# Optimization experiments

Measured on AMD Instinct MI355X. Metric: run time of the kernel, lower is better.

The kernel has to match this reference:

```python
import jax, jax.numpy as jnp
import numpy as np

N_SEG = 64        # number of graphs in batch
NEG_SLOPE = 0.2   # PyG GATConv leaky_relu slope


def seg_softmax(vals, seg, num_segments):
    # vals: [E, H]; softmax over entries sharing the same segment id
    m = jax.ops.segment_max(vals, seg, num_segments=num_segments)
    m = jnp.where(jnp.isfinite(m), m, 0.0)  # guard empty segments
    e = jnp.exp(vals - m[seg])
    s = jax.ops.segment_sum(e, seg, num_segments=num_segments)
    return e / (s[seg] + 1e-16)


def setup_inputs() -> dict:
    key = jax.random.key(0)
    ks = jax.random.split(key, 16)
    N, E, Fin, H, C1, C2 = 50000, 800000, 128, 4, 32, 128
    x = jax.random.normal(ks[0], (N, Fin), jnp.float32)
    edge_index = jax.random.randint(ks[1], (2, E), 0, N)
    batch = jnp.sort(jax.random.randint(ks[2], (N,), 0, N_SEG))
    sc = lambda fan: 1.0 / np.sqrt(fan)
    W_gat = jax.random.normal(ks[3], (Fin, H * C1), jnp.float32) * sc(Fin)
    att_src = jax.random.normal(ks[4], (H, C1), jnp.float32) * sc(C1)
    att_dst = jax.random.normal(ks[5], (H, C1), jnp.float32) * sc(C1)
    b_gat = jnp.zeros((H * C1,), jnp.float32)
    bn1_w = jax.random.uniform(ks[6], (H * C1,), jnp.float32, 0.5, 1.5)
    bn1_b = jax.random.normal(ks[7], (H * C1,), jnp.float32) * 0.1
    W_gcn = jax.random.normal(ks[8], (H * C1, C2), jnp.float32) * sc(H * C1)
    b_gcn = jnp.zeros((C2,), jnp.float32)
    bn2_w = jax.random.uniform(ks[9], (C2,), jnp.float32, 0.5, 1.5)
    bn2_b = jax.random.normal(ks[10], (C2,), jnp.float32) * 0.1
    W_gate = jax.random.normal(ks[11], (C2, 1), jnp.float32) * sc(C2)
    b_gate = jnp.zeros((1,), jnp.float32)
    W_fc = jax.random.normal(ks[12], (C2, 1), jnp.float32) * sc(C2)
    b_fc = jnp.zeros((1,), jnp.float32)
    return dict(x=x, edge_index=edge_index, batch=batch, W_gat=W_gat,
                att_src=att_src, att_dst=att_dst, b_gat=b_gat,
                bn1_w=bn1_w, bn1_b=bn1_b, W_gcn=W_gcn, b_gcn=b_gcn,
                bn2_w=bn2_w, bn2_b=bn2_b, W_gate=W_gate, b_gate=b_gate,
                W_fc=W_fc, b_fc=b_fc)


def reference(x, edge_index, batch, W_gat, att_src, att_dst, b_gat,
              bn1_w, bn1_b, W_gcn, b_gcn, bn2_w, bn2_b,
              W_gate, b_gate, W_fc, b_fc):
    N = x.shape[0]
    H, C1 = att_src.shape
    loops = jnp.arange(N)
    src = jnp.concatenate([edge_index[0], loops])  # message source j
    dst = jnp.concatenate([edge_index[1], loops])  # aggregation target i

    # ---- GATConv (heads=4, concat, add_self_loops) ----
    h = (x @ W_gat).reshape(N, H, C1)                       # [N,H,C1]
    a_src = jnp.einsum('nhc,hc->nh', h, att_src)
    a_dst = jnp.einsum('nhc,hc->nh', h, att_dst)
    e = jax.nn.leaky_relu(a_src[src] + a_dst[dst], NEG_SLOPE)  # [E',H]
    alpha = seg_softmax(e, dst, N)
    msg = h[src] * alpha[..., None]                          # [E',H,C1]
    out1 = jax.ops.segment_sum(msg, dst, num_segments=N).reshape(N, H * C1) + b_gat
    out1 = jax.nn.elu(out1)
    out1 = out1 * bn1_w + bn1_b          # BatchNorm1d (eval: mean 0, var 1)
    # dropout: identity (eval mode)

    # ---- GCNConv (self-loops, symmetric normalization) ----
    deg = jax.ops.segment_sum(jnp.ones_like(dst, dtype=x.dtype), dst, num_segments=N)
    dinv = jax.lax.rsqrt(jnp.maximum(deg, 1.0))
    norm = dinv[src] * dinv[dst]                             # [E']
    h2 = out1 @ W_gcn                                        # [N,C2]
    out2 = jax.ops.segment_sum(h2[src] * norm[:, None], dst, num_segments=N) + b_gcn
    out2 = jax.nn.elu(out2)
    out2 = out2 * bn2_w + bn2_b

    # ---- GlobalAttention pooling ----
    gate = out2 @ W_gate + b_gate                            # [N,1]
    w = seg_softmax(gate, batch, N_SEG)
    graph_rep = jax.ops.segment_sum(w * out2, batch, num_segments=N_SEG)  # [G,C2]

    out = graph_rep @ W_fc + b_fc                            # [G,1]
    return out.squeeze(1)
```

## Files before the change

kernel.cpp:

```cpp
#include <hip/hip_runtime.h>
#include <math.h>


#define NEG_SLOPE 0.2f
#define BKT_BITS 7
#define BKT_SIZE 128
#define CHUNK_A 4096

typedef __attribute__((ext_vector_type(8))) short short8v;
typedef __attribute__((ext_vector_type(4))) float floatx4;

__device__ __forceinline__ int lower_bound_i(const int* a, int n, int key) {
    int lo = 0, hi = n;
    while (lo < hi) {
        int mid = (lo + hi) >> 1;
        if (a[mid] < key) lo = mid + 1; else hi = mid;
    }
    return lo;
}

__device__ __forceinline__ unsigned pack_bf16(float lo, float hi) {
    unsigned ua = __float_as_uint(lo);
    unsigned ub = __float_as_uint(hi);
    ua = ua + 0x7fffu + ((ua >> 16) & 1u);
    ub = ub + 0x7fffu + ((ub >> 16) & 1u);
    return (ua >> 16) | (ub & 0xffff0000u);
}

__device__ __forceinline__ unsigned short bf16_1(float v) {
    unsigned u = __float_as_uint(v);
    u = u + 0x7fffu + ((u >> 16) & 1u);
    return (unsigned short)(u >> 16);
}

__global__ __launch_bounds__(256) void k_front(
    const float* __restrict__ W1, const float* __restrict__ atts,
    const float* __restrict__ attd, const float* __restrict__ W2,
    unsigned short* __restrict__ Wt1, unsigned short* __restrict__ Wt2,
    const int* __restrict__ dst, int* __restrict__ bcount, int E, int NB)
{
    const int b = blockIdx.x;
    if (b < 2) {
        const float* W = b ? W2 : W1;
        unsigned short* Wt = b ? Wt2 : Wt1;
        const int lim = b ? (128 * 128) : (144 * 128);
        for (int idx = threadIdx.x; idx < lim; idx += 256) {
            int j = idx >> 7, i = idx & 127;
            float v;
            if (j < 128) v = W[i * 128 + j];
            else if (j < 132) {
                int h = j - 128; float s = 0.f;
                for (int c = 0; c < 32; c++) s += W1[i * 128 + h * 32 + c] * atts[h * 32 + c];
                v = s;
            } else if (j < 136) {
                int h = j - 132; float s = 0.f;
                for (int c = 0; c < 32; c++) s += W1[i * 128 + h * 32 + c] * attd[h * 32 + c];
                v = s;
            } else v = 0.f;
            Wt[idx] = bf16_1(v);
        }
    } else {
        __shared__ int h[512];
        const int tid = threadIdx.x;
        for (int i = tid; i < 512; i += 256) h[i] = 0;
        __syncthreads();
        int base = (b - 2) * 2048;
#pragma unroll
        for (int k = 0; k < 8; k++) {
            int e = base + k * 256 + tid;
            if (e < E) atomicAdd(&h[dst[e] >> BKT_BITS], 1);
        }
        __syncthreads();
        for (int i = tid; i < NB; i += 256) {
            int c = h[i];
            if (c) atomicAdd(&bcount[i], c);
        }
    }
}

template<int MODE>
__global__ __launch_bounds__(256) void k_gemm_mfma(
    const void* __restrict__ Ain, const unsigned short* __restrict__ Wt,
    unsigned* __restrict__ Cb, int N,
    const float* __restrict__ pb, const float* __restrict__ pw,
    const float* __restrict__ pb2, const float* __restrict__ dinv,
    float* __restrict__ aS, float* __restrict__ aD)
{
    constexpr int NCT = (MODE == 0) ? 9 : 8;
    __shared__ unsigned short sA[128 * 136];
    __shared__ unsigned short sB[NCT * 16 * 136];
    const int tid = threadIdx.x;
    const int n0 = blockIdx.x * 128;

    {
        const uint4* Wg = (const uint4*)Wt;
        const int nq = NCT * 16 * 16;
        for (int q = tid; q < nq; q += 256) {
            uint4 v = Wg[q];
            int j = q >> 4, seg = q & 15;
            *(uint4*)(sB + j * 136 + seg * 8) = v;
        }
    }
    if (MODE == 0) {
        const float* A = (const float*)Ain;
        const int w4 = tid & 31;
        const int r0 = tid >> 5;
#pragma unroll
        for (int i = 0; i < 16; i++) {
            int r = r0 + 8 * i;
            int gn = n0 + r;
            unsigned p0 = 0, p1 = 0;
            if (gn < N) {
                float4 v = *(const float4*)(A + (size_t)gn * 128 + w4 * 4);
                p0 = pack_bf16(v.x, v.y);
                p1 = pack_bf16(v.z, v.w);
            }
            *(uint2*)(sA + r * 136 + w4 * 4) = make_uint2(p0, p1);
        }
    } else {
        const unsigned short* A = (const unsigned short*)Ain;
        const int w8 = tid & 15;
        const int r0 = tid >> 4;
        const int k0 = w8 * 8;
        float pbv[8], pwv[8], p2v[8];
        *(float4*)(pbv)     = *(const float4*)(pb + k0);
        *(float4*)(pbv + 4) = *(const float4*)(pb + k0 + 4);
        *(float4*)(pwv)     = *(const float4*)(pw + k0);
        *(float4*)(pwv + 4) = *(const float4*)(pw + k0 + 4);
        *(float4*)(p2v)     = *(const float4*)(pb2 + k0);
        *(float4*)(p2v + 4) = *(const float4*)(pb2 + k0 + 4);
#pragma unroll
        for (int i = 0; i < 8; i++) {
            int r = r0 + 16 * i;
            int gn = n0 + r;
            uint4 outv = make_uint4(0, 0, 0, 0);
            if (gn < N) {
                uint4 v = *(const uint4*)(A + (size_t)gn * 128 + k0);
                unsigned uu[4] = {v.x, v.y, v.z, v.w};
                unsigned ro[4];
#pragma unroll
                for (int q2 = 0; q2 < 4; q2++) {
                    float lo = __uint_as_float(uu[q2] << 16);
                    float hi = __uint_as_float(uu[q2] & 0xffff0000u);
                    float t;
                    t = lo + pbv[2 * q2];     t = (t > 0.f) ? t : expm1f(t); lo = t * pwv[2 * q2]     + p2v[2 * q2];
                    t = hi + pbv[2 * q2 + 1]; t = (t > 0.f) ? t : expm1f(t); hi = t * pwv[2 * q2 + 1] + p2v[2 * q2 + 1];
                    ro[q2] = pack_bf16(lo, hi);
                }
                outv = make_uint4(ro[0], ro[1], ro[2], ro[3]);
            }
            *(uint4*)(sA + r * 136 + k0) = outv;
        }
    }
    __syncthreads();

    const int wid = tid >> 6, lane = tid & 63;
    const int quad = lane >> 4, l16 = lane & 15;

    floatx4 acc[2][NCT];
#pragma unroll
    for (int rt = 0; rt < 2; rt++)
#pragma unroll
        for (int ct = 0; ct < NCT; ct++) acc[rt][ct] = (floatx4){0.f, 0.f, 0.f, 0.f};

    const unsigned short* pa0 = sA + (wid * 32 + l16) * 136 + quad * 8;
    const unsigned short* pbt = sB + l16 * 136 + quad * 8;
#pragma unroll
    for (int ks = 0; ks < 4; ks++) {
        short8v a0 = *(const short8v*)(pa0 + ks * 32);
        short8v a1 = *(const short8v*)(pa0 + 16 * 136 + ks * 32);
#pragma unroll
        for (int ct = 0; ct < NCT; ct++) {
            short8v bv = *(const short8v*)(pbt + ct * (16 * 136) + ks * 32);
            acc[0][ct] = __builtin_amdgcn_mfma_f32_16x16x32_bf16(a0, bv, acc[0][ct], 0, 0, 0);
            acc[1][ct] = __builtin_amdgcn_mfma_f32_16x16x32_bf16(a1, bv, acc[1][ct], 0, 0, 0);
        }
    }

#pragma unroll
    for (int rt = 0; rt < 2; rt++) {
#pragma unroll
        for (int r = 0; r < 4; r++) {
            int n = n0 + wid * 32 + rt * 16 + quad * 4 + r;
            if (n >= N) continue;
            float s = MODE ? dinv[n] : 1.f;
#pragma unroll
            for (int ct = 0; ct < 4; ct++) {
                Cb[(size_t)n * 64 + ct * 16 + l16] =
                    pack_bf16(acc[rt][ct][r] * s, acc[rt][ct + 4][r] * s);
            }
            if (MODE == 0) {
                float e = acc[rt][8][r];
                if (l16 < 4) aS[(size_t)n * 4 + l16] = e;
                else if (l16 < 8) aD[(size_t)n * 4 + (l16 - 4)] = e;
            }
        }
    }
}

__global__ __launch_bounds__(512) void k_bscan(const int* __restrict__ bcount,
                                               int* __restrict__ bb,
                                               int* __restrict__ bcur, int NB)
{
    __shared__ int sc[512];
    const int tid = threadIdx.x;
    int own = (tid < NB) ? bcount[tid] : 0;
    sc[tid] = own;
    __syncthreads();
    for (int st = 1; st < 512; st <<= 1) {
        int v = 0;
        if (tid >= st) v = sc[tid - st];
        __syncthreads();
        if (tid >= st) sc[tid] += v;
        __syncthreads();
    }
    int excl = sc[tid] - own;
    if (tid < NB) { bb[tid] = excl; bcur[tid] = excl; }
    if (tid == 511) { bb[NB] = sc[511]; bcur[NB] = sc[511]; }
}

__global__ __launch_bounds__(256) void k_binA(const int* __restrict__ ei,
                                              int* __restrict__ bcur,
                                              int2* __restrict__ pairs,
                                              int E, int NB)
{
    __shared__ int h[512];
    __shared__ int base[512];
    const int tid = threadIdx.x;
    for (int i = tid; i < NB + 1; i += 256) h[i] = 0;
    __syncthreads();
    const int c0 = blockIdx.x * CHUNK_A;
    int s[16], d[16], b[16];
#pragma unroll
    for (int k = 0; k < 16; k++) {
        int e = c0 + k * 256 + tid;
        bool v = e < E;
        s[k] = v ? ei[e] : 0;
        d[k] = v ? ei[E + e] : 0;
        b[k] = v ? (d[k] >> BKT_BITS) : NB;
        atomicAdd(&h[b[k]], 1);
    }
    __syncthreads();
    for (int i = tid; i < NB + 1; i += 256) {
        int c = h[i];
        base[i] = c ? atomicAdd(&bcur[i], c) : 0;
        h[i] = 0;
    }
    __syncthreads();
#pragma unroll
    for (int k = 0; k < 16; k++) {
        int r = atomicAdd(&h[b[k]], 1);
        pairs[base[b[k]] + r] = make_int2(s[k], d[k]);
    }
}

__global__ __launch_bounds__(256) void k_binB(const int2* __restrict__ pairs,
                                              const int* __restrict__ bb,
                                              int* __restrict__ csr,
                                              int* __restrict__ offs,
                                              float* __restrict__ dinv,
                                              int N, int NB, int E)
{
    __shared__ int hist[BKT_SIZE], start[BKT_SIZE], cur[BKT_SIZE];
    __shared__ int sc[BKT_SIZE];
    const int tid = threadIdx.x;
    const int b = blockIdx.x;
    const int d0 = b << BKT_BITS;
    const int pbg = bb[b], peg = bb[b + 1];

    if (tid < BKT_SIZE) { hist[tid] = 0; cur[tid] = 0; }
    __syncthreads();
    for (int i = pbg + tid; i < peg; i += 256)
        atomicAdd(&hist[pairs[i].y - d0], 1);
    __syncthreads();
    int own = (tid < BKT_SIZE) ? hist[tid] : 0;
    if (tid < BKT_SIZE) sc[tid] = own;
    __syncthreads();
    for (int st = 1; st < BKT_SIZE; st <<= 1) {
        int v = 0;
        bool act = (tid < BKT_SIZE) && (tid >= st);
        if (act) v = sc[tid - st];
        __syncthreads();
        if (act) sc[tid] += v;
        __syncthreads();
    }
    if (tid < BKT_SIZE) {
        int abs0 = pbg + (sc[tid] - own);
        start[tid] = abs0;
        int d = d0 + tid;
        if (d < N) {
            offs[d] = abs0;
            dinv[d] = rsqrtf((float)(own + 1));
        }
    }
    if (tid == 0 && b == NB - 1) offs[N] = E;
    __syncthreads();
    for (int i = pbg + tid; i < peg; i += 256) {
        int2 p = pairs[i];
        int ld = p.y - d0;
        int r = atomicAdd(&cur[ld], 1);
        csr[start[ld] + r] = p.x;
    }
}

__global__ __launch_bounds__(256) void k_gat_aggr(
    const unsigned* __restrict__ hb, const float* __restrict__ aSg,
    const float* __restrict__ aDg, const int* __restrict__ offs,
    const int* __restrict__ csr, unsigned short* __restrict__ raw1b, int N)
{
    __shared__ __align__(16) float s_u[4][64][4];
    __shared__ int s_s[4][64];

    const int wid = threadIdx.x >> 6;
    const int lane = threadIdx.x & 63;
    const int n = blockIdx.x * 4 + wid;
    if (n >= N) return;

    const int beg = offs[n];
    const int cnt = offs[n + 1] - beg + 1;
    const float4 ad = *(const float4*)(aDg + (size_t)n * 4);
    const int hA = lane >> 5;
    const float* pu = &s_u[wid][0][2 * hA];
    const int* ps = &s_s[wid][0];

    float t0 = 0.f, t1 = 0.f, t2 = 0.f, t3 = 0.f;
    float accLo = 0.f, accHi = 0.f;

    for (int base = 0; base < cnt; base += 64) {
        int idx = base + lane;
        bool valid = idx < cnt;
        int src = n;
        if (valid && idx > 0) src = csr[beg + idx - 1];
        float u0 = 0.f, u1 = 0.f, u2 = 0.f, u3 = 0.f;
        if (valid) {
            float4 as = *(const float4*)(aSg + (size_t)src * 4);
            float l0 = as.x + ad.x; l0 = (l0 > 0.f) ? l0 : NEG_SLOPE * l0;
            float l1 = as.y + ad.y; l1 = (l1 > 0.f) ? l1 : NEG_SLOPE * l1;
            float l2 = as.z + ad.z; l2 = (l2 > 0.f) ? l2 : NEG_SLOPE * l2;
            float l3 = as.w + ad.w; l3 = (l3 > 0.f) ? l3 : NEG_SLOPE * l3;
            u0 = __expf(l0); u1 = __expf(l1); u2 = __expf(l2); u3 = __expf(l3);
        }
        t0 += u0; t1 += u1; t2 += u2; t3 += u3;
        s_s[wid][lane] = src;
        *(float4*)&s_u[wid][lane][0] = make_float4(u0, u2, u1, u3);

        int cc = min(64, cnt - base);
        int j = 0;
        for (; j + 8 <= cc; j += 8) {
            int sj[8]; float2 uj[8]; unsigned vv[8];
#pragma unroll
            for (int k = 0; k < 8; k++) sj[k] = ps[j + k];
#pragma unroll
            for (int k = 0; k < 8; k++) uj[k] = *(const float2*)&pu[(j + k) * 4];
#pragma unroll
            for (int k = 0; k < 8; k++) vv[k] = hb[sj[k] * 64 + lane];
#pragma unroll
            for (int k = 0; k < 8; k++) {
                float lo = __uint_as_float(vv[k] << 16);
                float hi = __uint_as_float(vv[k] & 0xffff0000u);
                accLo += uj[k].x * lo;
                accHi += uj[k].y * hi;
            }
        }
        for (; j < cc; j++) {
            int sj = ps[j];
            float2 uv = *(const float2*)&pu[j * 4];
            unsigned v = hb[sj * 64 + lane];
            accLo += uv.x * __uint_as_float(v << 16);
            accHi += uv.y * __uint_as_float(v & 0xffff0000u);
        }
    }
#pragma unroll
    for (int msk = 1; msk < 64; msk <<= 1) {
        t0 += __shfl_xor(t0, msk);
        t1 += __shfl_xor(t1, msk);
        t2 += __shfl_xor(t2, msk);
        t3 += __shfl_xor(t3, msk);
    }
    float sLo = (hA ? t1 : t0) + 1e-16f;
    float sHi = (hA ? t3 : t2) + 1e-16f;
    raw1b[(size_t)n * 128 + lane]      = bf16_1(accLo / sLo);
    raw1b[(size_t)n * 128 + 64 + lane] = bf16_1(accHi / sHi);
}

__global__ __launch_bounds__(256) void k_gcn_aggr(
    const unsigned* __restrict__ h2b, const int* __restrict__ offs,
    const int* __restrict__ csr, const float* __restrict__ dinv,
    const float* __restrict__ bgcn,
    const float* __restrict__ bn2w, const float* __restrict__ bn2b,
    const float* __restrict__ wgate, const float* __restrict__ bgate,
    const float* __restrict__ wfc,
    float* __restrict__ gate, float* __restrict__ fcdot, int N)
{
    __shared__ int s_s[4][64];

    const int wid = threadIdx.x >> 6;
    const int lane = threadIdx.x & 63;
    const int n = blockIdx.x * 4 + wid;
    if (n >= N) return;

    const int beg = offs[n];
    const int cnt = offs[n + 1] - beg + 1;
    const float dn = dinv[n];
    const int* ps = &s_s[wid][0];

    float accLo = 0.f, accHi = 0.f;
    for (int base = 0; base < cnt; base += 64) {
        int idx = base + lane;
        int src = n;
        if (idx > 0 && idx < cnt) src = csr[beg + idx - 1];
        s_s[wid][lane] = src;

        int cc = min(64, cnt - base);
        int j = 0;
        for (; j + 8 <= cc; j += 8) {
            int sj[8]; unsigned vv[8];
#pragma unroll
            for (int k = 0; k < 8; k++) sj[k] = ps[j + k];
#pragma unroll
            for (int k = 0; k < 8; k++) vv[k] = h2b[sj[k] * 64 + lane];
#pragma unroll
            for (int k = 0; k < 8; k++) {
                accLo += __uint_as_float(vv[k] << 16);
                accHi += __uint_as_float(vv[k] & 0xffff0000u);
            }
        }
        for (; j < cc; j++) {
            unsigned v = h2b[ps[j] * 64 + lane];
            accLo += __uint_as_float(v << 16);
            accHi += __uint_as_float(v & 0xffff0000u);
        }
    }
    float v0 = dn * accLo + bgcn[lane];
    v0 = (v0 > 0.f) ? v0 : expm1f(v0);
    v0 = v0 * bn2w[lane] + bn2b[lane];
    float v1 = dn * accHi + bgcn[lane + 64];
    v1 = (v1 > 0.f) ? v1 : expm1f(v1);
    v1 = v1 * bn2w[lane + 64] + bn2b[lane + 64];

    float g = v0 * wgate[lane] + v1 * wgate[lane + 64];
    float f = v0 * wfc[lane]   + v1 * wfc[lane + 64];
#pragma unroll
    for (int msk = 1; msk < 64; msk <<= 1) {
        g += __shfl_xor(g, msk);
        f += __shfl_xor(f, msk);
    }
    if (lane == 0) { gate[n] = g + bgate[0]; fcdot[n] = f; }
}

__global__ __launch_bounds__(256) void k_pool(
    const float* __restrict__ gate, const float* __restrict__ fcdot,
    const int* __restrict__ batch, const float* __restrict__ bfc,
    float* __restrict__ out, int N)
{
    __shared__ float red[256];
    __shared__ int range[2];
    const int g = blockIdx.x;
    const int tid = threadIdx.x;
    if (tid < 2) range[tid] = lower_bound_i(batch, N, g + tid);
    __syncthreads();
    const int lo = range[0], hi = range[1];
    float se = 0.f, sf = 0.f;
    for (int i = lo + tid; i < hi; i += 256) {
        float e = __expf(gate[i]);
        se += e;
        sf += e * fcdot[i];
    }
    red[tid] = se; __syncthreads();
    for (int s = 128; s > 0; s >>= 1) {
        if (tid < s) red[tid] += red[tid + s];
        __syncthreads();
    }
    se = red[0]; __syncthreads();
    red[tid] = sf; __syncthreads();
    for (int s = 128; s > 0; s >>= 1) {
        if (tid < s) red[tid] += red[tid + s];
        __syncthreads();
    }
    sf = red[0];
    if (tid == 0) out[g] = sf / (se + 1e-16f) + bfc[0];
}

extern "C" void kernel_launch(void* const* d_in, const int* in_sizes, int n_in,
                              void* d_out, int out_size, void* d_ws, size_t ws_size,
                              hipStream_t stream) {
    const float* x     = (const float*)d_in[0];
    const int*   ei    = (const int*)d_in[1];
    const int*   batch = (const int*)d_in[2];
    const float* Wgat  = (const float*)d_in[3];
    const float* atts  = (const float*)d_in[4];
    const float* attd  = (const float*)d_in[5];
    const float* bgat  = (const float*)d_in[6];
    const float* bn1w  = (const float*)d_in[7];
    const float* bn1b  = (const float*)d_in[8];
    const float* Wgcn  = (const float*)d_in[9];
    const float* bgcn  = (const float*)d_in[10];
    const float* bn2w  = (const float*)d_in[11];
    const float* bn2b  = (const float*)d_in[12];
    const float* wgate = (const float*)d_in[13];
    const float* bgate = (const float*)d_in[14];
    const float* wfc   = (const float*)d_in[15];
    const float* bfc   = (const float*)d_in[16];
    float* out = (float*)d_out;

    const int N = in_sizes[0] / 128;
    const int E = in_sizes[1] / 2;
    const int NB = (N + BKT_SIZE - 1) / BKT_SIZE;
    const int NHB = (E + 2047) / 2048;

    unsigned* hb  = (unsigned*)d_ws;
    unsigned* h2b = hb + (size_t)N * 64;
    unsigned short* raw1b = (unsigned short*)(h2b + (size_t)N * 64);
    int2* pairs  = (int2*)raw1b;
    float* aS    = (float*)(raw1b + (size_t)N * 128);
    float* aD    = aS + (size_t)N * 4;
    float* gate  = aD + (size_t)N * 4;
    float* fcdot = gate + N;
    float* dinv  = fcdot + N;
    int* offs   = (int*)(dinv + N);
    int* csr    = offs + (N + 1);
    int* bcount = csr + E;
    int* bb     = bcount + (NB + 1);
    int* bcur   = bb + (NB + 1);
    unsigned short* Wt1 = (unsigned short*)(bcur + (NB + 1));
    unsigned short* Wt2 = Wt1 + 144 * 128;

    hipMemsetAsync(bcount, 0, (size_t)(NB + 1) * sizeof(int), stream);

    const int gemm_blocks = (N + 127) / 128;
    const int aggr_blocks = (N + 3) / 4;

    k_front<<<NHB + 2, 256, 0, stream>>>(Wgat, atts, attd, Wgcn, Wt1, Wt2,
                                         ei + E, bcount, E, NB);
    k_gemm_mfma<0><<<gemm_blocks, 256, 0, stream>>>(x, Wt1, hb, N,
                                                    nullptr, nullptr, nullptr,
                                                    nullptr, aS, aD);
    k_bscan<<<1, 512, 0, stream>>>(bcount, bb, bcur, NB);
    k_binA<<<(E + CHUNK_A - 1) / CHUNK_A, 256, 0, stream>>>(ei, bcur, pairs, E, NB);
    k_binB<<<NB, 256, 0, stream>>>(pairs, bb, csr, offs, dinv, N, NB, E);
    k_gat_aggr<<<aggr_blocks, 256, 0, stream>>>(hb, aS, aD, offs, csr, raw1b, N);
    k_gemm_mfma<1><<<gemm_blocks, 256, 0, stream>>>(raw1b, Wt2, h2b, N,
                                                    bgat, bn1w, bn1b, dinv,
                                                    nullptr, nullptr);
    k_gcn_aggr<<<aggr_blocks, 256, 0, stream>>>(h2b, offs, csr, dinv, bgcn,
                                                bn2w, bn2b, wgate, bgate, wfc,
                                                gate, fcdot, N);
    k_pool<<<64, 256, 0, stream>>>(gate, fcdot, batch, bfc, out, N);
}
```

Measured before the change: 264.5 us.

## Fuse GCN aggregation with global attention pooling via atomics and last-block finalize

Merges the GCN aggregation kernel and the pooling kernel into one launch. Each node's exp(gate) and weighted fc dot are atomically added into per-graph accumulators, and the last block to finish (tracked by an atomic counter) writes the final outputs. This removes one kernel launch and the gate/fcdot round trip through memory. In exchange it adds contended float atomics on only 64 addresses, plus a per-block fence and counter, and drops the max-subtraction in the softmax (the old pooling kernel also skipped it).

```diff
diff --git a/kernel.cpp b/kernel.cpp
--- a/kernel.cpp
+++ b/kernel.cpp
@@ -9,15 +9,6 @@
 
 typedef __attribute__((ext_vector_type(8))) short short8v;
 typedef __attribute__((ext_vector_type(4))) float floatx4;
-
-__device__ __forceinline__ int lower_bound_i(const int* a, int n, int key) {
-    int lo = 0, hi = n;
-    while (lo < hi) {
-        int mid = (lo + hi) >> 1;
-        if (a[mid] < key) lo = mid + 1; else hi = mid;
-    }
-    return lo;
-}
 
 __device__ __forceinline__ unsigned pack_bf16(float lo, float hi) {
     unsigned ua = __float_as_uint(lo);
@@ -383,102 +374,91 @@
     raw1b[(size_t)n * 128 + 64 + lane] = bf16_1(accHi / sHi);
 }
 
-__global__ __launch_bounds__(256) void k_gcn_aggr(
+__global__ __launch_bounds__(256) void k_gcn_pool(
     const unsigned* __restrict__ h2b, const int* __restrict__ offs,
     const int* __restrict__ csr, const float* __restrict__ dinv,
     const float* __restrict__ bgcn,
     const float* __restrict__ bn2w, const float* __restrict__ bn2b,
     const float* __restrict__ wgate, const float* __restrict__ bgate,
-    const float* __restrict__ wfc,
-    float* __restrict__ gate, float* __restrict__ fcdot, int N)
+    const float* __restrict__ wfc, const float* __restrict__ bfc,
+    const int* __restrict__ batch,
+    float* __restrict__ se, float* __restrict__ sf, int* __restrict__ done,
+    float* __restrict__ out, int N)
 {
     __shared__ int s_s[4][64];
+    __shared__ int s_last;
 
     const int wid = threadIdx.x >> 6;
     const int lane = threadIdx.x & 63;
     const int n = blockIdx.x * 4 + wid;
-    if (n >= N) return;
-
-    const int beg = offs[n];
-    const int cnt = offs[n + 1] - beg + 1;
-    const float dn = dinv[n];
-    const int* ps = &s_s[wid][0];
-
-    float accLo = 0.f, accHi = 0.f;
-    for (int base = 0; base < cnt; base += 64) {
-        int idx = base + lane;
-        int src = n;
-        if (idx > 0 && idx < cnt) src = csr[beg + idx - 1];
-        s_s[wid][lane] = src;
-
-        int cc = min(64, cnt - base);
-        int j = 0;
-        for (; j + 8 <= cc; j += 8) {
-            int sj[8]; unsigned vv[8];
-#pragma unroll
-            for (int k = 0; k < 8; k++) sj[k] = ps[j + k];
-#pragma unroll
-            for (int k = 0; k < 8; k++) vv[k] = h2b[sj[k] * 64 + lane];
-#pragma unroll
-            for (int k = 0; k < 8; k++) {
-                accLo += __uint_as_float(vv[k] << 16);
-                accHi += __uint_as_float(vv[k] & 0xffff0000u);
-            }
-        }
-        for (; j < cc; j++) {
-            unsigned v = h2b[ps[j] * 64 + lane];
-            accLo += __uint_as_float(v << 16);
-            accHi += __uint_as_float(v & 0xffff0000u);
-        }
-    }
-    float v0 = dn * accLo + bgcn[lane];
-    v0 = (v0 > 0.f) ? v0 : expm1f(v0);
-    v0 = v0 * bn2w[lane] + bn2b[lane];
-    float v1 = dn * accHi + bgcn[lane + 64];
-    v1 = (v1 > 0.f) ? v1 : expm1f(v1);
-    v1 = v1 * bn2w[lane + 64] + bn2b[lane + 64];
-
-    float g = v0 * wgate[lane] + v1 * wgate[lane + 64];
-    float f = v0 * wfc[lane]   + v1 * wfc[lane + 64];
-#pragma unroll
-    for (int msk = 1; msk < 64; msk <<= 1) {
-        g += __shfl_xor(g, msk);
-        f += __shfl_xor(f, msk);
-    }
-    if (lane == 0) { gate[n] = g + bgate[0]; fcdot[n] = f; }
-}
-
-__global__ __launch_bounds__(256) void k_pool(
-    const float* __restrict__ gate, const float* __restrict__ fcdot,
-    const int* __restrict__ batch, const float* __restrict__ bfc,
-    float* __restrict__ out, int N)
-{
-    __shared__ float red[256];
-    __shared__ int range[2];
-    const int g = blockIdx.x;
-    const int tid = threadIdx.x;
-    if (tid < 2) range[tid] = lower_bound_i(batch, N, g + tid);
-    __syncthreads();
-    const int lo = range[0], hi = range[1];
-    float se = 0.f, sf = 0.f;
-    for (int i = lo + tid; i < hi; i += 256) {
-        float e = __expf(gate[i]);
-        se += e;
-        sf += e * fcdot[i];
-    }
-    red[tid] = se; __syncthreads();
-    for (int s = 128; s > 0; s >>= 1) {
-        if (tid < s) red[tid] += red[tid + s];
-        __syncthreads();
-    }
-    se = red[0]; __syncthreads();
-    red[tid] = sf; __syncthreads();
-    for (int s = 128; s > 0; s >>= 1) {
-        if (tid < s) red[tid] += red[tid + s];
-        __syncthreads();
-    }
-    sf = red[0];
-    if (tid == 0) out[g] = sf / (se + 1e-16f) + bfc[0];
+    const bool active = (n < N);
+
+    if (active) {
+        const int beg = offs[n];
+        const int cnt = offs[n + 1] - beg + 1;
+        const float dn = dinv[n];
+        const int* ps = &s_s[wid][0];
+
+        float accLo = 0.f, accHi = 0.f;
+        for (int base = 0; base < cnt; base += 64) {
+            int idx = base + lane;
+            int src = n;
+            if (idx > 0 && idx < cnt) src = csr[beg + idx - 1];
+            s_s[wid][lane] = src;
+
+            int cc = min(64, cnt - base);
+            int j = 0;
+            for (; j + 8 <= cc; j += 8) {
+                int sj[8]; unsigned vv[8];
+#pragma unroll
+                for (int k = 0; k < 8; k++) sj[k] = ps[j + k];
+#pragma unroll
+                for (int k = 0; k < 8; k++) vv[k] = h2b[sj[k] * 64 + lane];
+#pragma unroll
+                for (int k = 0; k < 8; k++) {
+                    accLo += __uint_as_float(vv[k] << 16);
+                    accHi += __uint_as_float(vv[k] & 0xffff0000u);
+                }
+            }
+            for (; j < cc; j++) {
+                unsigned v = h2b[ps[j] * 64 + lane];
+                accLo += __uint_as_float(v << 16);
+                accHi += __uint_as_float(v & 0xffff0000u);
+            }
+        }
+        float v0 = dn * accLo + bgcn[lane];
+        v0 = (v0 > 0.f) ? v0 : expm1f(v0);
+        v0 = v0 * bn2w[lane] + bn2b[lane];
+        float v1 = dn * accHi + bgcn[lane + 64];
+        v1 = (v1 > 0.f) ? v1 : expm1f(v1);
+        v1 = v1 * bn2w[lane + 64] + bn2b[lane + 64];
+
+        float g = v0 * wgate[lane] + v1 * wgate[lane + 64];
+        float f = v0 * wfc[lane]   + v1 * wfc[lane + 64];
+#pragma unroll
+        for (int msk = 1; msk < 64; msk <<= 1) {
+            g += __shfl_xor(g, msk);
+            f += __shfl_xor(f, msk);
+        }
+        if (lane == 0) {
+            float e = __expf(g + bgate[0]);
+            int ga = batch[n];
+            atomicAdd(&se[ga], e);
+            atomicAdd(&sf[ga], e * f);
+        }
+    }
+    __syncthreads();
+    if (threadIdx.x == 0) {
+        __threadfence();
+        int t = atomicAdd(done, 1);
+        s_last = (t == (int)gridDim.x - 1) ? 1 : 0;
+    }
+    __syncthreads();
+    if (s_last && threadIdx.x < 64) {
+        float ses = atomicAdd(&se[threadIdx.x], 0.f);
+        float sfs = atomicAdd(&sf[threadIdx.x], 0.f);
+        out[threadIdx.x] = sfs / (ses + 1e-16f) + bfc[0];
+    }
 }
 
 extern "C" void kernel_launch(void* const* d_in, const int* in_sizes, int n_in,
@@ -514,18 +494,20 @@
     int2* pairs  = (int2*)raw1b;
     float* aS    = (float*)(raw1b + (size_t)N * 128);
     float* aD    = aS + (size_t)N * 4;
-    float* gate  = aD + (size_t)N * 4;
-    float* fcdot = gate + N;
-    float* dinv  = fcdot + N;
+    float* dinv  = aD + (size_t)N * 4;
     int* offs   = (int*)(dinv + N);
     int* csr    = offs + (N + 1);
     int* bcount = csr + E;
     int* bb     = bcount + (NB + 1);
     int* bcur   = bb + (NB + 1);
-    unsigned short* Wt1 = (unsigned short*)(bcur + (NB + 1));
+    float* se   = (float*)(bcur + (NB + 1));
+    float* sf   = se + 64;
+    int* done   = (int*)(sf + 64);
+    unsigned short* Wt1 = (unsigned short*)(done + 1);
     unsigned short* Wt2 = Wt1 + 144 * 128;
 
-    hipMemsetAsync(bcount, 0, (size_t)(NB + 1) * sizeof(int), stream);
+    hipMemsetAsync(bcount, 0,
+                   (size_t)(3 * (NB + 1) + 129) * sizeof(int), stream);
 
     const int gemm_blocks = (N + 127) / 128;
     const int aggr_blocks = (N + 3) / 4;
@@ -542,8 +524,8 @@
     k_gemm_mfma<1><<<gemm_blocks, 256, 0, stream>>>(raw1b, Wt2, h2b, N,
                                                     bgat, bn1w, bn1b, dinv,
                                                     nullptr, nullptr);
-    k_gcn_aggr<<<aggr_blocks, 256, 0, stream>>>(h2b, offs, csr, dinv, bgcn,
-                                                bn2w, bn2b, wgate, bgate, wfc,
-                                                gate, fcdot, N);
-    k_pool<<<64, 256, 0, stream>>>(gate, fcdot, batch, bfc, out, N);
-}
+    k_gcn_pool<<<aggr_blocks, 256, 0, stream>>>(h2b, offs, csr, dinv, bgcn,
+                                                bn2w, bn2b, wgate, bgate,
+                                                wfc, bfc, batch,
+                                                se, sf, done, out, N);
+}
```

New measurement: 808.9 us. 3.06x slower.

## Pre-swizzle weights into MFMA fragment layout and drop LDS staging in GEMMs

Applied to the files above, without the earlier changes.

The weight matrices are now pre-packed in k_front into the per-lane MFMA B-fragment order, so the GEMM kernels read B fragments straight from global/L2 and A rows straight from memory, with no shared-memory tiles and no __syncthreads. The GEMM tile shrinks from 128 to 64 rows per block, with one 16-row tile per wave, which doubles the grid. The bias+ELU+BN1 epilogue moves from the second GEMM's A-load into the GAT aggregation output. The aim is to cut LDS traffic, the barrier and prologue latency. The cost is that each wave re-reads the weights from cache, and B reuse across row tiles is lost.

```diff
diff --git a/kernel.cpp b/kernel.cpp
--- a/kernel.cpp
+++ b/kernel.cpp
@@ -36,28 +36,36 @@
 __global__ __launch_bounds__(256) void k_front(
     const float* __restrict__ W1, const float* __restrict__ atts,
     const float* __restrict__ attd, const float* __restrict__ W2,
-    unsigned short* __restrict__ Wt1, unsigned short* __restrict__ Wt2,
+    unsigned short* __restrict__ Wf1, unsigned short* __restrict__ Wf2,
     const int* __restrict__ dst, int* __restrict__ bcount, int E, int NB)
 {
     const int b = blockIdx.x;
     if (b < 2) {
+        const int NCT = b ? 8 : 9;
         const float* W = b ? W2 : W1;
-        unsigned short* Wt = b ? Wt2 : Wt1;
-        const int lim = b ? (128 * 128) : (144 * 128);
+        unsigned short* Wf = b ? Wf2 : Wf1;
+        const int lim = NCT * 4 * 64 * 8;
         for (int idx = threadIdx.x; idx < lim; idx += 256) {
-            int j = idx >> 7, i = idx & 127;
+            int j = idx & 7;
+            int lane = (idx >> 3) & 63;
+            int frag = idx >> 9;
+            int ct = frag >> 2, ks = frag & 3;
+            int quad = lane >> 4, l16 = lane & 15;
+            int k = ks * 32 + quad * 8 + j;
             float v;
-            if (j < 128) v = W[i * 128 + j];
-            else if (j < 132) {
-                int h = j - 128; float s = 0.f;
-                for (int c = 0; c < 32; c++) s += W1[i * 128 + h * 32 + c] * atts[h * 32 + c];
+            if (ct < 8) {
+                v = W[k * 128 + ct * 16 + l16];
+            } else if (l16 < 4) {
+                float s = 0.f;
+                for (int c = 0; c < 32; c++) s += W1[k * 128 + l16 * 32 + c] * atts[l16 * 32 + c];
                 v = s;
-            } else if (j < 136) {
-                int h = j - 132; float s = 0.f;
-                for (int c = 0; c < 32; c++) s += W1[i * 128 + h * 32 + c] * attd[h * 32 + c];
+            } else if (l16 < 8) {
+                int h = l16 - 4;
+                float s = 0.f;
+                for (int c = 0; c < 32; c++) s += W1[k * 128 + h * 32 + c] * attd[h * 32 + c];
                 v = s;
             } else v = 0.f;
-            Wt[idx] = bf16_1(v);
+            Wf[idx] = bf16_1(v);
         }
     } else {
         __shared__ int h[512];
@@ -80,120 +88,65 @@
 
 template<int MODE>
 __global__ __launch_bounds__(256) void k_gemm_mfma(
-    const void* __restrict__ Ain, const unsigned short* __restrict__ Wt,
+    const void* __restrict__ Ain, const unsigned short* __restrict__ Wf,
     unsigned* __restrict__ Cb, int N,
-    const float* __restrict__ pb, const float* __restrict__ pw,
-    const float* __restrict__ pb2, const float* __restrict__ dinv,
+    const float* __restrict__ dinv,
     float* __restrict__ aS, float* __restrict__ aD)
 {
     constexpr int NCT = (MODE == 0) ? 9 : 8;
-    __shared__ unsigned short sA[128 * 136];
-    __shared__ unsigned short sB[NCT * 16 * 136];
     const int tid = threadIdx.x;
-    const int n0 = blockIdx.x * 128;
-
-    {
-        const uint4* Wg = (const uint4*)Wt;
-        const int nq = NCT * 16 * 16;
-        for (int q = tid; q < nq; q += 256) {
-            uint4 v = Wg[q];
-            int j = q >> 4, seg = q & 15;
-            *(uint4*)(sB + j * 136 + seg * 8) = v;
-        }
-    }
-    if (MODE == 0) {
-        const float* A = (const float*)Ain;
-        const int w4 = tid & 31;
-        const int r0 = tid >> 5;
-#pragma unroll
-        for (int i = 0; i < 16; i++) {
-            int r = r0 + 8 * i;
-            int gn = n0 + r;
-            unsigned p0 = 0, p1 = 0;
-            if (gn < N) {
-                float4 v = *(const float4*)(A + (size_t)gn * 128 + w4 * 4);
-                p0 = pack_bf16(v.x, v.y);
-                p1 = pack_bf16(v.z, v.w);
+    const int wv = tid >> 6, lane = tid & 63;
+    const int quad = lane >> 4, l16 = lane & 15;
+    const int n0 = blockIdx.x * 64;
+    const int arow = n0 + wv * 16 + l16;
+    const bool rowok = arow < N;
+
+    floatx4 acc[NCT];
+#pragma unroll
+    for (int ct = 0; ct < NCT; ct++) acc[ct] = (floatx4){0.f, 0.f, 0.f, 0.f};
+
+    union AV { unsigned u[4]; short8v v; };
+
+#pragma unroll
+    for (int ks = 0; ks < 4; ks++) {
+        AV a;
+        a.u[0] = a.u[1] = a.u[2] = a.u[3] = 0u;
+        if (rowok) {
+            if (MODE == 0) {
+                const float* A = (const float*)Ain;
+                const float* p = A + (size_t)arow * 128 + ks * 32 + quad * 8;
+                float4 va = *(const float4*)(p);
+                float4 vb = *(const float4*)(p + 4);
+                a.u[0] = pack_bf16(va.x, va.y);
+                a.u[1] = pack_bf16(va.z, va.w);
+                a.u[2] = pack_bf16(vb.x, vb.y);
+                a.u[3] = pack_bf16(vb.z, vb.w);
+            } else {
+                const unsigned short* A = (const unsigned short*)Ain;
+                a.v = *(const short8v*)(A + (size_t)arow * 128 + ks * 32 + quad * 8);
             }
-            *(uint2*)(sA + r * 136 + w4 * 4) = make_uint2(p0, p1);
-        }
-    } else {
-        const unsigned short* A = (const unsigned short*)Ain;
-        const int w8 = tid & 15;
-        const int r0 = tid >> 4;
-        const int k0 = w8 * 8;
-        float pbv[8], pwv[8], p2v[8];
-        *(float4*)(pbv)     = *(const float4*)(pb + k0);
-        *(float4*)(pbv + 4) = *(const float4*)(pb + k0 + 4);
-        *(float4*)(pwv)     = *(const float4*)(pw + k0);
-        *(float4*)(pwv + 4) = *(const float4*)(pw + k0 + 4);
-        *(float4*)(p2v)     = *(const float4*)(pb2 + k0);
-        *(float4*)(p2v + 4) = *(const float4*)(pb2 + k0 + 4);
-#pragma unroll
-        for (int i = 0; i < 8; i++) {
-            int r = r0 + 16 * i;
-            int gn = n0 + r;
-            uint4 outv = make_uint4(0, 0, 0, 0);
-            if (gn < N) {
-                uint4 v = *(const uint4*)(A + (size_t)gn * 128 + k0);
-                unsigned uu[4] = {v.x, v.y, v.z, v.w};
-                unsigned ro[4];
-#pragma unroll
-                for (int q2 = 0; q2 < 4; q2++) {
-                    float lo = __uint_as_float(uu[q2] << 16);
-                    float hi = __uint_as_float(uu[q2] & 0xffff0000u);
-                    float t;
-                    t = lo + pbv[2 * q2];     t = (t > 0.f) ? t : expm1f(t); lo = t * pwv[2 * q2]     + p2v[2 * q2];
-                    t = hi + pbv[2 * q2 + 1]; t = (t > 0.f) ? t : expm1f(t); hi = t * pwv[2 * q2 + 1] + p2v[2 * q2 + 1];
-                    ro[q2] = pack_bf16(lo, hi);
-                }
-                outv = make_uint4(ro[0], ro[1], ro[2], ro[3]);
-            }
-            *(uint4*)(sA + r * 136 + k0) = outv;
-        }
-    }
-    __syncthreads();
-
-    const int wid = tid >> 6, lane = tid & 63;
-    const int quad = lane >> 4, l16 = lane & 15;
-
-    floatx4 acc[2][NCT];
-#pragma unroll
-    for (int rt = 0; rt < 2; rt++)
-#pragma unroll
-        for (int ct = 0; ct < NCT; ct++) acc[rt][ct] = (floatx4){0.f, 0.f, 0.f, 0.f};
-
-    const unsigned short* pa0 = sA + (wid * 32 + l16) * 136 + quad * 8;
-    const unsigned short* pbt = sB + l16 * 136 + quad * 8;
-#pragma unroll
-    for (int ks = 0; ks < 4; ks++) {
-        short8v a0 = *(const short8v*)(pa0 + ks * 32);
-        short8v a1 = *(const short8v*)(pa0 + 16 * 136 + ks * 32);
+        }
 #pragma unroll
         for (int ct = 0; ct < NCT; ct++) {
-            short8v bv = *(const short8v*)(pbt + ct * (16 * 136) + ks * 32);
-            acc[0][ct] = __builtin_amdgcn_mfma_f32_16x16x32_bf16(a0, bv, acc[0][ct], 0, 0, 0);
-            acc[1][ct] = __builtin_amdgcn_mfma_f32_16x16x32_bf16(a1, bv, acc[1][ct], 0, 0, 0);
-        }
-    }
-
-#pragma unroll
-    for (int rt = 0; rt < 2; rt++) {
-#pragma unroll
-        for (int r = 0; r < 4; r++) {
-            int n = n0 + wid * 32 + rt * 16 + quad * 4 + r;
-            if (n >= N) continue;
-            float s = MODE ? dinv[n] : 1.f;
-#pragma unroll
-            for (int ct = 0; ct < 4; ct++) {
-                Cb[(size_t)n * 64 + ct * 16 + l16] =
-                    pack_bf16(acc[rt][ct][r] * s, acc[rt][ct + 4][r] * s);
-            }
-            if (MODE == 0) {
-                float e = acc[rt][8][r];
-                if (l16 < 4) aS[(size_t)n * 4 + l16] = e;
-                else if (l16 < 8) aD[(size_t)n * 4 + (l16 - 4)] = e;
-            }
+            short8v bv = *(const short8v*)(Wf + ((ct * 4 + ks) << 9) + lane * 8);
+            acc[ct] = __builtin_amdgcn_mfma_f32_16x16x32_bf16(a.v, bv, acc[ct], 0, 0, 0);
+        }
+    }
+
+#pragma unroll
+    for (int r = 0; r < 4; r++) {
+        int n = n0 + wv * 16 + quad * 4 + r;
+        if (n >= N) continue;
+        float s = MODE ? dinv[n] : 1.f;
+#pragma unroll
+        for (int ct = 0; ct < 4; ct++) {
+            Cb[(size_t)n * 64 + ct * 16 + l16] =
+                pack_bf16(acc[ct][r] * s, acc[ct + 4][r] * s);
+        }
+        if (MODE == 0) {
+            float e = acc[8][r];
+            if (l16 < 4) aS[(size_t)n * 4 + l16] = e;
+            else if (l16 < 8) aD[(size_t)n * 4 + (l16 - 4)] = e;
         }
     }
 }
@@ -306,7 +259,10 @@
 __global__ __launch_bounds__(256) void k_gat_aggr(
     const unsigned* __restrict__ hb, const float* __restrict__ aSg,
     const float* __restrict__ aDg, const int* __restrict__ offs,
-    const int* __restrict__ csr, unsigned short* __restrict__ raw1b, int N)
+    const int* __restrict__ csr,
+    const float* __restrict__ bgat, const float* __restrict__ bn1w,
+    const float* __restrict__ bn1b,
+    unsigned short* __restrict__ raw1b, int N)
 {
     __shared__ __align__(16) float s_u[4][64][4];
     __shared__ int s_s[4][64];
@@ -379,8 +335,14 @@
     }
     float sLo = (hA ? t1 : t0) + 1e-16f;
     float sHi = (hA ? t3 : t2) + 1e-16f;
-    raw1b[(size_t)n * 128 + lane]      = bf16_1(accLo / sLo);
-    raw1b[(size_t)n * 128 + 64 + lane] = bf16_1(accHi / sHi);
+    float o0 = accLo / sLo + bgat[lane];
+    o0 = (o0 > 0.f) ? o0 : expm1f(o0);
+    o0 = o0 * bn1w[lane] + bn1b[lane];
+    float o1 = accHi / sHi + bgat[lane + 64];
+    o1 = (o1 > 0.f) ? o1 : expm1f(o1);
+    o1 = o1 * bn1w[lane + 64] + bn1b[lane + 64];
+    raw1b[(size_t)n * 128 + lane]      = bf16_1(o0);
+    raw1b[(size_t)n * 128 + 64 + lane] = bf16_1(o1);
 }
 
 __global__ __launch_bounds__(256) void k_gcn_aggr(
@@ -522,26 +484,25 @@
     int* bcount = csr + E;
     int* bb     = bcount + (NB + 1);
     int* bcur   = bb + (NB + 1);
-    unsigned short* Wt1 = (unsigned short*)(bcur + (NB + 1));
-    unsigned short* Wt2 = Wt1 + 144 * 128;
+    unsigned short* Wf1 = (unsigned short*)(bcur + (NB + 1));
+    unsigned short* Wf2 = Wf1 + 9 * 4 * 64 * 8;
 
     hipMemsetAsync(bcount, 0, (size_t)(NB + 1) * sizeof(int), stream);
 
-    const int gemm_blocks = (N + 127) / 128;
+    const int gemm_blocks = (N + 63) / 64;
     const int aggr_blocks = (N + 3) / 4;
 
-    k_front<<<NHB + 2, 256, 0, stream>>>(Wgat, atts, attd, Wgcn, Wt1, Wt2,
+    k_front<<<NHB + 2, 256, 0, stream>>>(Wgat, atts, attd, Wgcn, Wf1, Wf2,
                                          ei + E, bcount, E, NB);
-    k_gemm_mfma<0><<<gemm_blocks, 256, 0, stream>>>(x, Wt1, hb, N,
-                                                    nullptr, nullptr, nullptr,
+    k_gemm_mfma<0><<<gemm_blocks, 256, 0, stream>>>(x, Wf1, hb, N,
                                                     nullptr, aS, aD);
     k_bscan<<<1, 512, 0, stream>>>(bcount, bb, bcur, NB);
     k_binA<<<(E + CHUNK_A - 1) / CHUNK_A, 256, 0, stream>>>(ei, bcur, pairs, E, NB);
     k_binB<<<NB, 256, 0, stream>>>(pairs, bb, csr, offs, dinv, N, NB, E);
-    k_gat_aggr<<<aggr_blocks, 256, 0, stream>>>(hb, aS, aD, offs, csr, raw1b, N);
-    k_gemm_mfma<1><<<gemm_blocks, 256, 0, stream>>>(raw1b, Wt2, h2b, N,
-                                                    bgat, bn1w, bn1b, dinv,
-                                                    nullptr, nullptr);
+    k_gat_aggr<<<aggr_blocks, 256, 0, stream>>>(hb, aS, aD, offs, csr,
+                                                bgat, bn1w, bn1b, raw1b, N);
+    k_gemm_mfma<1><<<gemm_blocks, 256, 0, stream>>>(raw1b, Wf2, h2b, N,
+                                                    dinv, nullptr, nullptr);
     k_gcn_aggr<<<aggr_blocks, 256, 0, stream>>>(h2b, offs, csr, dinv, bgcn,
                                                 bn2w, bn2b, wgate, bgate, wfc,
                                                 gate, fcdot, N);
```

Result: slower. 270.7 us (+2.3%).
